# Kernel tuning notes

Measured on AMD Instinct MI355X. Metric: run time of the kernel, lower is better.

## Reference

```python
import jax, jax.numpy as jnp
import numpy as np

N = 16384      # nodes
E = 262144     # edges (avg degree 16)
R = 9          # relation types
D_IN = 384     # embed_size
D_H = 768      # hidden_size
N_CLASSES = 5


def setup_inputs() -> dict:
    key = jax.random.key(0)
    ks = jax.random.split(key, 11)
    s = 0.02
    return {
        "x": jax.random.normal(ks[0], (N, D_IN), jnp.float32),
        "edge_index": jax.random.randint(ks[1], (2, E), 0, N, dtype=jnp.int64)
        if jax.config.jax_enable_x64 else jax.random.randint(ks[1], (2, E), 0, N).astype(jnp.int32),
        "edge_type": jax.random.randint(ks[2], (E,), 0, R).astype(jnp.int32),
        "rel_W": jax.random.normal(ks[3], (R, D_H, D_IN), jnp.float32) * s,
        "rel_b": jax.random.normal(ks[4], (R, D_H), jnp.float32) * s,
        "norm_constants": jnp.ones((R,), jnp.float32),
        "mp_lin_W": jax.random.normal(ks[5], (D_H, D_H), jnp.float32) * s,
        "mp_lin_b": jax.random.normal(ks[6], (D_H,), jnp.float32) * s,
        "mp_self_W": jax.random.normal(ks[7], (D_H, D_H), jnp.float32) * s,
        "mp_self_b": jax.random.normal(ks[8], (D_H,), jnp.float32) * s,
        "out_W": jax.random.normal(ks[9], (N_CLASSES, D_H), jnp.float32) * s,
        "out_b": jax.random.normal(ks[10], (N_CLASSES,), jnp.float32) * s,
    }


def reference(x, edge_index, edge_type, rel_W, rel_b, norm_constants,
              mp_lin_W, mp_lin_b, mp_self_W, mp_self_b, out_W, out_b):
    n = x.shape[0]
    src = edge_index[0]  # j : message source (x_j)
    dst = edge_index[1]  # i : aggregation target

    # --- RelationAwareMP ---
    # edge_weights[i, j] from x @ x.T, computed per edge (identical math)
    ew = jnp.einsum('ed,ed->e', x[dst], x[src])                  # [E]
    norm = ew / norm_constants[edge_type]                        # [E]
    # per-relation linear applied to all nodes, then gathered per edge
    h = jnp.einsum('nd,rhd->rnh', x, rel_W) + rel_b[:, None, :]  # [R,N,H]
    msg = h[edge_type, src]                                      # [E,H]
    aggr = jax.ops.segment_sum(norm[:, None] * msg, dst, num_segments=n)
    x1 = jax.nn.relu(aggr)                                       # [N,H]

    # --- MP (add aggregation + self transform) ---
    self_x = x1 @ mp_self_W.T + mp_self_b
    hm = x1 @ mp_lin_W.T + mp_lin_b
    aggr2 = jax.ops.segment_sum(hm[src], dst, num_segments=n)
    x2 = jax.nn.relu(aggr2 + self_x)                             # [N,H]

    # --- readout ---
    pooled = x2.mean(axis=0)                                     # [H]
    return pooled @ out_W.T + out_b                              # [N_CLASSES]
```

## Files before the change

kernel.cpp:

```cpp
#include <hip/hip_runtime.h>

typedef unsigned char  u8;
typedef unsigned short u16;
typedef unsigned int   u32;

#define NN   16384
#define EE   262144
#define RR   9
#define DIN  384
#define DH   768
#define KSU  3456
#define KS   3488
#define NPB  8
#define PCOP 16

typedef float  f32x4 __attribute__((ext_vector_type(4)));
typedef float  f32x2 __attribute__((ext_vector_type(2)));
typedef __bf16 b16x8 __attribute__((ext_vector_type(8)));

__device__ __forceinline__ u16 f2bf(float f){
  u32 u = __builtin_bit_cast(u32, f);
  u += 0x7fffu + ((u >> 16) & 1u);
  return (u16)(u >> 16);
}
__device__ __forceinline__ float bf2f(u16 h){
  u32 u = ((u32)h) << 16;
  return __builtin_bit_cast(float, u);
}
__device__ __forceinline__ void gll16(const void* g, void* l){
  __builtin_amdgcn_global_load_lds((const __attribute__((address_space(1))) void*)g,
                                   (__attribute__((address_space(3))) void*)l, 16, 0, 0);
}

__global__ void k_count(const int* __restrict__ dst, int* __restrict__ counts){
  const int e = blockIdx.x*256 + threadIdx.x;
  if (e < EE) atomicAdd(&counts[dst[e]], 1);
}

__global__ __launch_bounds__(1024) void k_scan(const int* __restrict__ counts,
                                               int* __restrict__ starts,
                                               int* __restrict__ cursor){
  __shared__ int tot[1024];
  const int t = threadIdx.x;
  int loc[16]; int s = 0;
  #pragma unroll
  for (int j=0;j<16;j++){ loc[j] = counts[t*16+j]; s += loc[j]; }
  tot[t] = s;
  __syncthreads();
  for (int o=1;o<1024;o<<=1){
    int v = (t>=o) ? tot[t-o] : 0;
    __syncthreads();
    tot[t] += v;
    __syncthreads();
  }
  int run = tot[t] - s;
  #pragma unroll
  for (int j=0;j<16;j++){ starts[t*16+j] = run; cursor[t*16+j] = run; run += loc[j]; }
  if (t == 1023) starts[NN] = run;
}

__global__ void k_place(const int* __restrict__ src, const int* __restrict__ dst,
                        const int* __restrict__ et, int* __restrict__ cursor,
                        int* __restrict__ srcp, int* __restrict__ rp){
  const int e = blockIdx.x*256 + threadIdx.x;
  if (e < EE){
    const int p = atomicAdd(&cursor[dst[e]], 1);
    srcp[p] = src[e];
    rp[p]   = et[e];
  }
}

__global__ void k_convW1(const float* __restrict__ rW, const float* __restrict__ rb,
                         u16* __restrict__ Wst){
  const int hh = blockIdx.y;
  const int k  = blockIdx.x*256 + threadIdx.x;
  if (k >= KS) return;
  float v;
  if (k < KSU){ const int r = k / DIN; const int d = k - r*DIN;
                v = rW[((long)r*DH + hh)*DIN + d]; }
  else if (k < KSU + RR){ const int r = k - KSU; v = rb[(long)r*DH + hh]; }
  else v = 0.f;
  Wst[(long)hh*KS + k] = f2bf(v);
}

__global__ void k_convW2(const float* __restrict__ lW, const float* __restrict__ sW,
                         u16* __restrict__ WB){
  const int idx = blockIdx.x*256 + threadIdx.x;
  const float v = (idx < DH*DH) ? lW[idx] : sW[idx - DH*DH];
  WB[idx] = f2bf(v);
}

__global__ __launch_bounds__(256, 3) void k_phase1f(const float* __restrict__ x,
                                                    const int* __restrict__ srcp,
                                                    const int* __restrict__ rp,
                                                    const float* __restrict__ nc,
                                                    const int* __restrict__ starts,
                                                    u16* __restrict__ s){
  const int wv = threadIdx.x >> 6;
  const int l  = threadIdx.x & 63;
  const int i  = blockIdx.x*4 + wv;
  const float* xdp = x + (long)i*DIN;
  const f32x2 xd0 = *(const f32x2*)(xdp + 2*l);
  const f32x2 xd1 = *(const f32x2*)(xdp + 128 + 2*l);
  const f32x2 xd2 = *(const f32x2*)(xdp + 256 + 2*l);
  float acc[RR][6];
  float cacc[RR];
  #pragma unroll
  for (int r=0;r<RR;r++){
    cacc[r] = 0.f;
    #pragma unroll
    for (int j=0;j<6;j++) acc[r][j] = 0.f;
  }
  const int e0 = starts[i], e1 = starts[i+1];
  f32x2 A0={0.f,0.f}, A1={0.f,0.f}, A2={0.f,0.f};
  f32x2 B0={0.f,0.f}, B1={0.f,0.f}, B2={0.f,0.f};
  int rA = 0, rB = 0;
  if (e0 < e1){
    const float* xs = x + (long)srcp[e0]*DIN;
    A0 = *(const f32x2*)(xs + 2*l);
    A1 = *(const f32x2*)(xs + 128 + 2*l);
    A2 = *(const f32x2*)(xs + 256 + 2*l);
    rA = rp[e0];
  }
  if (e0+1 < e1){
    const float* xs = x + (long)srcp[e0+1]*DIN;
    B0 = *(const f32x2*)(xs + 2*l);
    B1 = *(const f32x2*)(xs + 128 + 2*l);
    B2 = *(const f32x2*)(xs + 256 + 2*l);
    rB = rp[e0+1];
  }
  for (int p=e0; p<e1; p+=2){
    const f32x2 a0=A0, a1=A1, a2=A2;
    const f32x2 b0=B0, b1=B1, b2=B2;
    const int ra = rA, rb = rB;
    const bool hb = (p+1 < e1);
    if (p+2 < e1){
      const float* xs = x + (long)srcp[p+2]*DIN;
      A0 = *(const f32x2*)(xs + 2*l);
      A1 = *(const f32x2*)(xs + 128 + 2*l);
      A2 = *(const f32x2*)(xs + 256 + 2*l);
      rA = rp[p+2];
    }
    if (p+3 < e1){
      const float* xs = x + (long)srcp[p+3]*DIN;
      B0 = *(const f32x2*)(xs + 2*l);
      B1 = *(const f32x2*)(xs + 128 + 2*l);
      B2 = *(const f32x2*)(xs + 256 + 2*l);
      rB = rp[p+3];
    }
    float pa = xd0.x*a0.x + xd0.y*a0.y + xd1.x*a1.x + xd1.y*a1.y
             + xd2.x*a2.x + xd2.y*a2.y;
    float pb = xd0.x*b0.x + xd0.y*b0.y + xd1.x*b1.x + xd1.y*b1.y
             + xd2.x*b2.x + xd2.y*b2.y;
    #pragma unroll
    for (int o=32;o;o>>=1){
      pa += __shfl_xor(pa, o);
      pb += __shfl_xor(pb, o);
    }
    #define UPD(R,P,c0,c1,c2) { cacc[R] += P; \
      acc[R][0] += P*c0.x; acc[R][1] += P*c0.y; acc[R][2] += P*c1.x; \
      acc[R][3] += P*c1.y; acc[R][4] += P*c2.x; acc[R][5] += P*c2.y; }
    switch (ra){
      case 0: UPD(0,pa,a0,a1,a2); break; case 1: UPD(1,pa,a0,a1,a2); break;
      case 2: UPD(2,pa,a0,a1,a2); break; case 3: UPD(3,pa,a0,a1,a2); break;
      case 4: UPD(4,pa,a0,a1,a2); break; case 5: UPD(5,pa,a0,a1,a2); break;
      case 6: UPD(6,pa,a0,a1,a2); break; case 7: UPD(7,pa,a0,a1,a2); break;
      default: UPD(8,pa,a0,a1,a2); break;
    }
    if (hb){
      switch (rb){
        case 0: UPD(0,pb,b0,b1,b2); break; case 1: UPD(1,pb,b0,b1,b2); break;
        case 2: UPD(2,pb,b0,b1,b2); break; case 3: UPD(3,pb,b0,b1,b2); break;
        case 4: UPD(4,pb,b0,b1,b2); break; case 5: UPD(5,pb,b0,b1,b2); break;
        case 6: UPD(6,pb,b0,b1,b2); break; case 7: UPD(7,pb,b0,b1,b2); break;
        default: UPD(8,pb,b0,b1,b2); break;
      }
    }
    #undef UPD
  }
  u16* srow = s + (long)i*KS;
  #pragma unroll
  for (int r=0;r<RR;r++){
    const float inv = 1.0f / nc[r];
    #pragma unroll
    for (int seg=0;seg<3;seg++){
      const u32 pk = (u32)f2bf(acc[r][seg*2]*inv)
                   | ((u32)f2bf(acc[r][seg*2+1]*inv) << 16);
      ((u32*)(srow + r*DIN + seg*128))[l] = pk;
    }
  }
  float cv = 0.f;
  #pragma unroll
  for (int r=0;r<RR;r++) cv = (l == r) ? cacc[r] : cv;
  if (l < 32){
    const float invl = (l < RR) ? 1.0f/nc[l] : 0.f;
    srow[KSU + l] = f2bf(l < RR ? cv*invl : 0.f);
  }
}

template<int MODE>
__global__ __launch_bounds__(256, 2)
void k_gemm_bt(const u16* __restrict__ A, const u16* __restrict__ B,
               int M, int N, int K,
               u16* __restrict__ O0, u16* __restrict__ O1,
               const float* __restrict__ b0, const float* __restrict__ b1)
{
  __shared__ __align__(16) u16 As[128*32];
  __shared__ __align__(16) u16 Bs[128*32];
  const int t  = threadIdx.x;
  const int wv = t >> 6;
  const int ln = t & 63;
  const int wm = wv >> 1, wn = wv & 1;
  const long m0 = (long)blockIdx.x * 128;
  const long n0 = (long)blockIdx.y * 128;

  const int srow  = ln >> 2;
  const int skcol = (ln & 3) * 8;

  f32x4 acc[4][4];
  #pragma unroll
  for (int i=0;i<4;i++)
    #pragma unroll
    for (int j=0;j<4;j++) acc[i][j] = {0.f,0.f,0.f,0.f};

  const int fr = ln & 15, fq = ln >> 4;
  const int nk = K >> 5;
  for (int kb=0; kb<nk; ++kb){
    const long k0 = (long)kb * 32;
    #pragma unroll
    for (int q=0;q<2;q++){
      const int seg = wv*2 + q;
      const int row = seg*16 + srow;
      gll16(A + (m0 + row)*(long)K + k0 + skcol, &As[seg*512]);
      gll16(B + (n0 + row)*(long)K + k0 + skcol, &Bs[seg*512]);
    }
    __syncthreads();
    b16x8 av[4], bv[4];
    #pragma unroll
    for (int i=0;i<4;i++){
      av[i] = *(const b16x8*)&As[(wm*64 + i*16 + fr)*32 + fq*8];
      bv[i] = *(const b16x8*)&Bs[(wn*64 + i*16 + fr)*32 + fq*8];
    }
    #pragma unroll
    for (int i=0;i<4;i++)
      #pragma unroll
      for (int j=0;j<4;j++)
        acc[i][j] = __builtin_amdgcn_mfma_f32_16x16x32_bf16(av[i], bv[j], acc[i][j], 0, 0, 0);
    __syncthreads();
  }

  #pragma unroll
  for (int i=0;i<4;i++){
    #pragma unroll
    for (int j=0;j<4;j++){
      #pragma unroll
      for (int r=0;r<4;r++){
        const long m = m0 + wm*64 + i*16 + fq*4 + r;
        const long n = n0 + wn*64 + j*16 + fr;
        float v = acc[i][j][r];
        if (MODE == 0){
          v = v > 0.f ? v : 0.f;
          O0[m*DH + n] = f2bf(v);
        } else {
          if (n < DH) O0[m*DH + n]      = f2bf(v + b0[n]);
          else        O1[m*DH + (n-DH)] = f2bf(v + b1[n-DH]);
        }
      }
    }
  }
}

__global__ __launch_bounds__(128) void k_phase2(const u16* __restrict__ hm,
                                                const u16* __restrict__ sfx,
                                                const int* __restrict__ srcp,
                                                const int* __restrict__ starts,
                                                float* __restrict__ pooledP){
  const int t  = threadIdx.x;
  const int i0 = blockIdx.x * NPB;
  int p = starts[i0];
  const int pend = starts[i0 + NPB];
  u32 C0=0u, C1=0u, C2=0u;
  if (p < pend){
    const u32* hr = (const u32*)(hm + (long)srcp[p]*DH);
    C0 = hr[t]; C1 = hr[t+128]; C2 = hr[t+256];
  }
  float pool[6] = {0.f,0.f,0.f,0.f,0.f,0.f};
  for (int i=i0; i<i0+NPB; ++i){
    const int e1 = starts[i+1];
    float a[6] = {0.f,0.f,0.f,0.f,0.f,0.f};
    while (p < e1){
      const u32 d0=C0, d1=C1, d2=C2;
      if (p+1 < pend){
        const u32* hr = (const u32*)(hm + (long)srcp[p+1]*DH);
        C0 = hr[t]; C1 = hr[t+128]; C2 = hr[t+256];
      }
      a[0] += bf2f((u16)d0); a[1] += bf2f((u16)(d0>>16));
      a[2] += bf2f((u16)d1); a[3] += bf2f((u16)(d1>>16));
      a[4] += bf2f((u16)d2); a[5] += bf2f((u16)(d2>>16));
      ++p;
    }
    const u32* sr = (const u32*)(sfx + (long)i*DH);
    const u32 s0 = sr[t], s1 = sr[t+128], s2 = sr[t+256];
    float v;
    v = a[0] + bf2f((u16)s0);        pool[0] += v > 0.f ? v : 0.f;
    v = a[1] + bf2f((u16)(s0>>16));  pool[1] += v > 0.f ? v : 0.f;
    v = a[2] + bf2f((u16)s1);        pool[2] += v > 0.f ? v : 0.f;
    v = a[3] + bf2f((u16)(s1>>16));  pool[3] += v > 0.f ? v : 0.f;
    v = a[4] + bf2f((u16)s2);        pool[4] += v > 0.f ? v : 0.f;
    v = a[5] + bf2f((u16)(s2>>16));  pool[5] += v > 0.f ? v : 0.f;
  }
  float* pd = pooledP + (blockIdx.x & (PCOP-1)) * DH;
  atomicAdd(&pd[2*t],       pool[0]);
  atomicAdd(&pd[2*t+1],     pool[1]);
  atomicAdd(&pd[256+2*t],   pool[2]);
  atomicAdd(&pd[256+2*t+1], pool[3]);
  atomicAdd(&pd[512+2*t],   pool[4]);
  atomicAdd(&pd[512+2*t+1], pool[5]);
}

__global__ __launch_bounds__(256) void k_final(const float* __restrict__ pooledP,
                                               const float* __restrict__ oW,
                                               const float* __restrict__ ob,
                                               float* __restrict__ out){
  __shared__ float ps[DH];
  __shared__ float red[256];
  const int t = threadIdx.x;
  for (int h=t; h<DH; h+=256){
    float s = 0.f;
    #pragma unroll
    for (int c=0;c<PCOP;c++) s += pooledP[c*DH + h];
    ps[h] = s;
  }
  __syncthreads();
  for (int c=0;c<5;c++){
    float p = 0.f;
    for (int h=t; h<DH; h+=256) p += ps[h]*oW[c*DH + h];
    red[t] = p; __syncthreads();
    for (int o=128;o;o>>=1){ if (t<o) red[t]+=red[t+o]; __syncthreads(); }
    if (t == 0) out[c] = red[0]*(1.f/(float)NN) + ob[c];
    __syncthreads();
  }
}

extern "C" void kernel_launch(void* const* d_in, const int* in_sizes, int n_in,
                              void* d_out, int out_size, void* d_ws, size_t ws_size,
                              hipStream_t stream)
{
  (void)in_sizes; (void)n_in; (void)out_size; (void)ws_size;
  const float* x     = (const float*)d_in[0];
  const int*   ei    = (const int*)  d_in[1];
  const int*   et    = (const int*)  d_in[2];
  const float* relW  = (const float*)d_in[3];
  const float* relb  = (const float*)d_in[4];
  const float* nc    = (const float*)d_in[5];
  const float* linW  = (const float*)d_in[6];
  const float* linb  = (const float*)d_in[7];
  const float* selfW = (const float*)d_in[8];
  const float* selfb = (const float*)d_in[9];
  const float* outW  = (const float*)d_in[10];
  const float* outb  = (const float*)d_in[11];
  float* out = (float*)d_out;

  u8* w = (u8*)d_ws;
  int*   counts = (int*)(w + 0);
  int*   starts = (int*)(w + 65536);
  int*   cursor = (int*)(w + 131328);
  int*   srcp   = (int*)(w + 196864);
  int*   rp     = (int*)(w + 2294016);
  u16*   Wst    = (u16*)(w + 4391168);
  u16*   WB     = (u16*)(w + 9748736);
  u16*   x1     = (u16*)(w + 12108032);
  u16*   S      = (u16*)(w + 37276928);
  u16*   hm     = S;
  u16*   sfx    = (u16*)(w + 37276928 + 25165824);
  float* pooledP = (float*)(w + 37276928 + 50331648);

  const int* esrc = ei;
  const int* edst = ei + EE;

  hipMemsetAsync(counts, 0, NN*sizeof(int), stream);

  k_count <<<EE/256, 256, 0, stream>>>(edst, counts);
  k_scan  <<<1, 1024, 0, stream>>>(counts, starts, cursor);
  k_place <<<EE/256, 256, 0, stream>>>(esrc, edst, et, cursor, srcp, rp);
  k_convW1<<<dim3(14, DH), 256, 0, stream>>>(relW, relb, Wst);
  k_convW2<<<(2*DH*DH)/256, 256, 0, stream>>>(linW, selfW, WB);
  k_phase1f<<<NN/4, 256, 0, stream>>>(x, srcp, rp, nc, starts, S);
  k_gemm_bt<0><<<dim3(NN/128, DH/128), 256, 0, stream>>>(
      S, Wst, NN, DH, KS, x1, (u16*)nullptr, (const float*)nullptr, (const float*)nullptr);
  hipMemsetAsync(pooledP, 0, PCOP*DH*sizeof(float), stream);
  k_gemm_bt<1><<<dim3(NN/128, 2*DH/128), 256, 0, stream>>>(
      x1, WB, NN, 2*DH, DH, hm, sfx, linb, selfb);
  k_phase2<<<NN/NPB, 128, 0, stream>>>(hm, sfx, srcp, starts, pooledP);
  k_final <<<1, 256, 0, stream>>>(pooledP, outW, outb, out);
}
```

Before: 494.9 us.

## Pack edge src/type, deepen gather prefetch, DPP reductions, swap GEMM grid order

Packs each edge's source index and relation type into one int, which halves the CSR index reads. The phase-1 gather now prefetches four edges ahead and reduces its dot products with DPP and ds_swizzle instead of a full shuffle chain. Phase 2 now handles four nodes per block and runs an eight-deep prefetch pipeline across node boundaries. The GEMM grid is transposed so that N tiles vary fastest, which should improve reuse of A tiles in L2, and its occupancy hint is raised to 3. The extra prefetch depth raises register pressure, and the packing assumes the source index fits in 14 bits and the relation type in 4.

```diff
diff --git a/kernel.cpp b/kernel.cpp
--- a/kernel.cpp
+++ b/kernel.cpp
@@ -11,7 +11,7 @@
 #define DH   768
 #define KSU  3456
 #define KS   3488
-#define NPB  8
+#define NPB  4
 #define PCOP 16
 
 typedef float  f32x4 __attribute__((ext_vector_type(4)));
@@ -30,6 +30,14 @@
 __device__ __forceinline__ void gll16(const void* g, void* l){
   __builtin_amdgcn_global_load_lds((const __attribute__((address_space(1))) void*)g,
                                    (__attribute__((address_space(3))) void*)l, 16, 0, 0);
+}
+template<int N> __device__ __forceinline__ float dppror(float v){
+  return __builtin_bit_cast(float,
+    __builtin_amdgcn_update_dpp(0, __builtin_bit_cast(int, v), 0x120+N, 0xF, 0xF, true));
+}
+__device__ __forceinline__ float swz16(float v){
+  return __builtin_bit_cast(float,
+    __builtin_amdgcn_ds_swizzle(__builtin_bit_cast(int, v), 0x401F));
 }
 
 __global__ void k_count(const int* __restrict__ dst, int* __restrict__ counts){
@@ -61,12 +69,11 @@
 
 __global__ void k_place(const int* __restrict__ src, const int* __restrict__ dst,
                         const int* __restrict__ et, int* __restrict__ cursor,
-                        int* __restrict__ srcp, int* __restrict__ rp){
+                        int* __restrict__ sp){
   const int e = blockIdx.x*256 + threadIdx.x;
   if (e < EE){
     const int p = atomicAdd(&cursor[dst[e]], 1);
-    srcp[p] = src[e];
-    rp[p]   = et[e];
+    sp[p] = (int)(((u32)et[e] << 28) | (u32)src[e]);
   }
 }
 
@@ -91,8 +98,7 @@
 }
 
 __global__ __launch_bounds__(256, 3) void k_phase1f(const float* __restrict__ x,
-                                                    const int* __restrict__ srcp,
-                                                    const int* __restrict__ rp,
+                                                    const int* __restrict__ sp,
                                                     const float* __restrict__ nc,
                                                     const int* __restrict__ starts,
                                                     u16* __restrict__ s){
@@ -112,72 +118,52 @@
     for (int j=0;j<6;j++) acc[r][j] = 0.f;
   }
   const int e0 = starts[i], e1 = starts[i+1];
-  f32x2 A0={0.f,0.f}, A1={0.f,0.f}, A2={0.f,0.f};
-  f32x2 B0={0.f,0.f}, B1={0.f,0.f}, B2={0.f,0.f};
-  int rA = 0, rB = 0;
-  if (e0 < e1){
-    const float* xs = x + (long)srcp[e0]*DIN;
-    A0 = *(const f32x2*)(xs + 2*l);
-    A1 = *(const f32x2*)(xs + 128 + 2*l);
-    A2 = *(const f32x2*)(xs + 256 + 2*l);
-    rA = rp[e0];
-  }
-  if (e0+1 < e1){
-    const float* xs = x + (long)srcp[e0+1]*DIN;
-    B0 = *(const f32x2*)(xs + 2*l);
-    B1 = *(const f32x2*)(xs + 128 + 2*l);
-    B2 = *(const f32x2*)(xs + 256 + 2*l);
-    rB = rp[e0+1];
-  }
-  for (int p=e0; p<e1; p+=2){
-    const f32x2 a0=A0, a1=A1, a2=A2;
-    const f32x2 b0=B0, b1=B1, b2=B2;
-    const int ra = rA, rb = rB;
-    const bool hb = (p+1 < e1);
-    if (p+2 < e1){
-      const float* xs = x + (long)srcp[p+2]*DIN;
-      A0 = *(const f32x2*)(xs + 2*l);
-      A1 = *(const f32x2*)(xs + 128 + 2*l);
-      A2 = *(const f32x2*)(xs + 256 + 2*l);
-      rA = rp[p+2];
-    }
-    if (p+3 < e1){
-      const float* xs = x + (long)srcp[p+3]*DIN;
-      B0 = *(const f32x2*)(xs + 2*l);
-      B1 = *(const f32x2*)(xs + 128 + 2*l);
-      B2 = *(const f32x2*)(xs + 256 + 2*l);
-      rB = rp[p+3];
-    }
-    float pa = xd0.x*a0.x + xd0.y*a0.y + xd1.x*a1.x + xd1.y*a1.y
-             + xd2.x*a2.x + xd2.y*a2.y;
-    float pb = xd0.x*b0.x + xd0.y*b0.y + xd1.x*b1.x + xd1.y*b1.y
-             + xd2.x*b2.x + xd2.y*b2.y;
-    #pragma unroll
-    for (int o=32;o;o>>=1){
-      pa += __shfl_xor(pa, o);
-      pb += __shfl_xor(pb, o);
-    }
-    #define UPD(R,P,c0,c1,c2) { cacc[R] += P; \
+  f32x2 Aa={0.f,0.f},Ab={0.f,0.f},Ac={0.f,0.f};
+  f32x2 Ba={0.f,0.f},Bb={0.f,0.f},Bc={0.f,0.f};
+  f32x2 Ca={0.f,0.f},Cb={0.f,0.f},Cc={0.f,0.f};
+  f32x2 Da={0.f,0.f},Db={0.f,0.f},Dc={0.f,0.f};
+  u32 qA=0,qB=0,qC=0,qD=0;
+  #define LDE(S, QQ, IDX) { const int pe_=(IDX); if (pe_ < e1){ QQ = (u32)sp[pe_]; \
+      const float* xs_ = x + (long)(QQ & 0x3FFFu)*DIN; \
+      S##a = *(const f32x2*)(xs_ + 2*l); \
+      S##b = *(const f32x2*)(xs_ + 128 + 2*l); \
+      S##c = *(const f32x2*)(xs_ + 256 + 2*l); } }
+  LDE(A,qA,e0) LDE(B,qB,e0+1) LDE(C,qC,e0+2) LDE(D,qD,e0+3)
+  #define DOT(u0,u1,u2) (xd0.x*u0.x + xd0.y*u0.y + xd1.x*u1.x + xd1.y*u1.y \
+                       + xd2.x*u2.x + xd2.y*u2.y)
+  #define UPD(R,P,c0,c1,c2) { cacc[R] += P; \
       acc[R][0] += P*c0.x; acc[R][1] += P*c0.y; acc[R][2] += P*c1.x; \
       acc[R][3] += P*c1.y; acc[R][4] += P*c2.x; acc[R][5] += P*c2.y; }
-    switch (ra){
-      case 0: UPD(0,pa,a0,a1,a2); break; case 1: UPD(1,pa,a0,a1,a2); break;
-      case 2: UPD(2,pa,a0,a1,a2); break; case 3: UPD(3,pa,a0,a1,a2); break;
-      case 4: UPD(4,pa,a0,a1,a2); break; case 5: UPD(5,pa,a0,a1,a2); break;
-      case 6: UPD(6,pa,a0,a1,a2); break; case 7: UPD(7,pa,a0,a1,a2); break;
-      default: UPD(8,pa,a0,a1,a2); break;
-    }
-    if (hb){
-      switch (rb){
-        case 0: UPD(0,pb,b0,b1,b2); break; case 1: UPD(1,pb,b0,b1,b2); break;
-        case 2: UPD(2,pb,b0,b1,b2); break; case 3: UPD(3,pb,b0,b1,b2); break;
-        case 4: UPD(4,pb,b0,b1,b2); break; case 5: UPD(5,pb,b0,b1,b2); break;
-        case 6: UPD(6,pb,b0,b1,b2); break; case 7: UPD(7,pb,b0,b1,b2); break;
-        default: UPD(8,pb,b0,b1,b2); break;
-      }
-    }
-    #undef UPD
-  }
+  #define SW(RQ,P,c0,c1,c2) switch (RQ){ \
+      case 0: UPD(0,P,c0,c1,c2); break; case 1: UPD(1,P,c0,c1,c2); break; \
+      case 2: UPD(2,P,c0,c1,c2); break; case 3: UPD(3,P,c0,c1,c2); break; \
+      case 4: UPD(4,P,c0,c1,c2); break; case 5: UPD(5,P,c0,c1,c2); break; \
+      case 6: UPD(6,P,c0,c1,c2); break; case 7: UPD(7,P,c0,c1,c2); break; \
+      default: UPD(8,P,c0,c1,c2); break; }
+  for (int p=e0; p<e1; p+=4){
+    const f32x2 a0=Aa,a1=Ab,a2=Ac, b0=Ba,b1=Bb,b2=Bc;
+    const f32x2 c0=Ca,c1=Cb,c2=Cc, d0=Da,d1=Db,d2=Dc;
+    const u32 qa=qA, qb=qB, qc=qC, qd=qD;
+    const bool h1 = p+1<e1, h2 = p+2<e1, h3 = p+3<e1;
+    LDE(A,qA,p+4) LDE(B,qB,p+5) LDE(C,qC,p+6) LDE(D,qD,p+7)
+    float pa = DOT(a0,a1,a2), pb = DOT(b0,b1,b2);
+    float pc = DOT(c0,c1,c2), pd = DOT(d0,d1,d2);
+    pa += dppror<1>(pa); pb += dppror<1>(pb); pc += dppror<1>(pc); pd += dppror<1>(pd);
+    pa += dppror<2>(pa); pb += dppror<2>(pb); pc += dppror<2>(pc); pd += dppror<2>(pd);
+    pa += dppror<4>(pa); pb += dppror<4>(pb); pc += dppror<4>(pc); pd += dppror<4>(pd);
+    pa += dppror<8>(pa); pb += dppror<8>(pb); pc += dppror<8>(pc); pd += dppror<8>(pd);
+    pa += swz16(pa); pb += swz16(pb); pc += swz16(pc); pd += swz16(pd);
+    pa += __shfl_xor(pa,32); pb += __shfl_xor(pb,32);
+    pc += __shfl_xor(pc,32); pd += __shfl_xor(pd,32);
+    SW(qa>>28, pa, a0,a1,a2);
+    if (h1){ SW(qb>>28, pb, b0,b1,b2); }
+    if (h2){ SW(qc>>28, pc, c0,c1,c2); }
+    if (h3){ SW(qd>>28, pd, d0,d1,d2); }
+  }
+  #undef LDE
+  #undef DOT
+  #undef UPD
+  #undef SW
   u16* srow = s + (long)i*KS;
   #pragma unroll
   for (int r=0;r<RR;r++){
@@ -199,7 +185,7 @@
 }
 
 template<int MODE>
-__global__ __launch_bounds__(256, 2)
+__global__ __launch_bounds__(256, 3)
 void k_gemm_bt(const u16* __restrict__ A, const u16* __restrict__ B,
                int M, int N, int K,
                u16* __restrict__ O0, u16* __restrict__ O1,
@@ -211,8 +197,8 @@
   const int wv = t >> 6;
   const int ln = t & 63;
   const int wm = wv >> 1, wn = wv & 1;
-  const long m0 = (long)blockIdx.x * 128;
-  const long n0 = (long)blockIdx.y * 128;
+  const long m0 = (long)blockIdx.y * 128;
+  const long n0 = (long)blockIdx.x * 128;
 
   const int srow  = ln >> 2;
   const int skcol = (ln & 3) * 8;
@@ -272,50 +258,64 @@
 
 __global__ __launch_bounds__(128) void k_phase2(const u16* __restrict__ hm,
                                                 const u16* __restrict__ sfx,
-                                                const int* __restrict__ srcp,
+                                                const int* __restrict__ sp,
                                                 const int* __restrict__ starts,
                                                 float* __restrict__ pooledP){
   const int t  = threadIdx.x;
   const int i0 = blockIdx.x * NPB;
-  int p = starts[i0];
+  const int p0 = starts[i0];
   const int pend = starts[i0 + NPB];
-  u32 C0=0u, C1=0u, C2=0u;
-  if (p < pend){
-    const u32* hr = (const u32*)(hm + (long)srcp[p]*DH);
-    C0 = hr[t]; C1 = hr[t+128]; C2 = hr[t+256];
-  }
-  float pool[6] = {0.f,0.f,0.f,0.f,0.f,0.f};
-  for (int i=i0; i<i0+NPB; ++i){
-    const int e1 = starts[i+1];
-    float a[6] = {0.f,0.f,0.f,0.f,0.f,0.f};
-    while (p < e1){
-      const u32 d0=C0, d1=C1, d2=C2;
-      if (p+1 < pend){
-        const u32* hr = (const u32*)(hm + (long)srcp[p+1]*DH);
-        C0 = hr[t]; C1 = hr[t+128]; C2 = hr[t+256];
-      }
-      a[0] += bf2f((u16)d0); a[1] += bf2f((u16)(d0>>16));
-      a[2] += bf2f((u16)d1); a[3] += bf2f((u16)(d1>>16));
-      a[4] += bf2f((u16)d2); a[5] += bf2f((u16)(d2>>16));
-      ++p;
-    }
-    const u32* sr = (const u32*)(sfx + (long)i*DH);
-    const u32 s0 = sr[t], s1 = sr[t+128], s2 = sr[t+256];
-    float v;
-    v = a[0] + bf2f((u16)s0);        pool[0] += v > 0.f ? v : 0.f;
-    v = a[1] + bf2f((u16)(s0>>16));  pool[1] += v > 0.f ? v : 0.f;
-    v = a[2] + bf2f((u16)s1);        pool[2] += v > 0.f ? v : 0.f;
-    v = a[3] + bf2f((u16)(s1>>16));  pool[3] += v > 0.f ? v : 0.f;
-    v = a[4] + bf2f((u16)s2);        pool[4] += v > 0.f ? v : 0.f;
-    v = a[5] + bf2f((u16)(s2>>16));  pool[5] += v > 0.f ? v : 0.f;
-  }
+  u32 sf00,sf01,sf02, sf10,sf11,sf12, sf20,sf21,sf22, sf30,sf31,sf32;
+  { const u32* sr = (const u32*)(sfx + (long)(i0+0)*DH); sf00=sr[t]; sf01=sr[t+128]; sf02=sr[t+256]; }
+  { const u32* sr = (const u32*)(sfx + (long)(i0+1)*DH); sf10=sr[t]; sf11=sr[t+128]; sf12=sr[t+256]; }
+  { const u32* sr = (const u32*)(sfx + (long)(i0+2)*DH); sf20=sr[t]; sf21=sr[t+128]; sf22=sr[t+256]; }
+  { const u32* sr = (const u32*)(sfx + (long)(i0+3)*DH); sf30=sr[t]; sf31=sr[t+128]; sf32=sr[t+256]; }
+  u32 A0=0,A1=0,A2=0,B0=0,B1=0,B2=0,C0=0,C1=0,C2=0,D0=0,D1=0,D2=0;
+  u32 E0=0,E1=0,E2=0,F0=0,F1=0,F2=0,G0=0,G1=0,G2=0,H0=0,H1=0,H2=0;
+  #define PLD(S, IDX) { const int nf_=(IDX); if (nf_ < pend){ \
+      const u32* hr_ = (const u32*)(hm + (long)(((u32)sp[nf_]) & 0x3FFFu)*DH); \
+      S##0=hr_[t]; S##1=hr_[t+128]; S##2=hr_[t+256]; } }
+  PLD(A,p0)   PLD(B,p0+1) PLD(C,p0+2) PLD(D,p0+3)
+  PLD(E,p0+4) PLD(F,p0+5) PLD(G,p0+6) PLD(H,p0+7)
+  float a0=0.f,a1=0.f,a2=0.f,a3=0.f,a4=0.f,a5=0.f;
+  float q0=0.f,q1=0.f,q2=0.f,q3=0.f,q4=0.f,q5=0.f;
+  int i = i0;
+  int e1 = starts[i0+1];
+  #define FLUSH(K) { float v_; \
+    v_=a0+bf2f((u16)sf##K##0);        q0+=fmaxf(v_,0.f); \
+    v_=a1+bf2f((u16)(sf##K##0>>16));  q1+=fmaxf(v_,0.f); \
+    v_=a2+bf2f((u16)sf##K##1);        q2+=fmaxf(v_,0.f); \
+    v_=a3+bf2f((u16)(sf##K##1>>16));  q3+=fmaxf(v_,0.f); \
+    v_=a4+bf2f((u16)sf##K##2);        q4+=fmaxf(v_,0.f); \
+    v_=a5+bf2f((u16)(sf##K##2>>16));  q5+=fmaxf(v_,0.f); \
+    a0=a1=a2=a3=a4=a5=0.f; }
+  #define FLUSHI { switch (i - i0){ case 0: FLUSH(0); break; case 1: FLUSH(1); break; \
+                   case 2: FLUSH(2); break; default: FLUSH(3); break; } }
+  while (i < i0+NPB && e1 == p0){ FLUSHI; ++i; e1 = (i < i0+NPB) ? starts[i+1] : 0x7fffffff; }
+  #define STEP(S, K) { const int pe_ = base + K; if (pe_ < pend){ \
+      const u32 d0_=S##0, d1_=S##1, d2_=S##2; \
+      PLD(S, pe_ + 8); \
+      a0+=bf2f((u16)d0_); a1+=bf2f((u16)(d0_>>16)); \
+      a2+=bf2f((u16)d1_); a3+=bf2f((u16)(d1_>>16)); \
+      a4+=bf2f((u16)d2_); a5+=bf2f((u16)(d2_>>16)); \
+      while (i < i0+NPB && pe_+1 == e1){ FLUSHI; ++i; \
+        e1 = (i < i0+NPB) ? starts[i+1] : 0x7fffffff; } } }
+  for (int base = p0; base < pend; base += 8){
+    STEP(A,0) STEP(B,1) STEP(C,2) STEP(D,3)
+    STEP(E,4) STEP(F,5) STEP(G,6) STEP(H,7)
+  }
+  while (i < i0+NPB){ FLUSHI; ++i; }
+  #undef PLD
+  #undef FLUSH
+  #undef FLUSHI
+  #undef STEP
   float* pd = pooledP + (blockIdx.x & (PCOP-1)) * DH;
-  atomicAdd(&pd[2*t],       pool[0]);
-  atomicAdd(&pd[2*t+1],     pool[1]);
-  atomicAdd(&pd[256+2*t],   pool[2]);
-  atomicAdd(&pd[256+2*t+1], pool[3]);
-  atomicAdd(&pd[512+2*t],   pool[4]);
-  atomicAdd(&pd[512+2*t+1], pool[5]);
+  atomicAdd(&pd[2*t],       q0);
+  atomicAdd(&pd[2*t+1],     q1);
+  atomicAdd(&pd[256+2*t],   q2);
+  atomicAdd(&pd[256+2*t+1], q3);
+  atomicAdd(&pd[512+2*t],   q4);
+  atomicAdd(&pd[512+2*t+1], q5);
 }
 
 __global__ __launch_bounds__(256) void k_final(const float* __restrict__ pooledP,
@@ -366,7 +366,6 @@
   int*   starts = (int*)(w + 65536);
   int*   cursor = (int*)(w + 131328);
   int*   srcp   = (int*)(w + 196864);
-  int*   rp     = (int*)(w + 2294016);
   u16*   Wst    = (u16*)(w + 4391168);
   u16*   WB     = (u16*)(w + 9748736);
   u16*   x1     = (u16*)(w + 12108032);
@@ -382,14 +381,14 @@
 
   k_count <<<EE/256, 256, 0, stream>>>(edst, counts);
   k_scan  <<<1, 1024, 0, stream>>>(counts, starts, cursor);
-  k_place <<<EE/256, 256, 0, stream>>>(esrc, edst, et, cursor, srcp, rp);
+  k_place <<<EE/256, 256, 0, stream>>>(esrc, edst, et, cursor, srcp);
   k_convW1<<<dim3(14, DH), 256, 0, stream>>>(relW, relb, Wst);
   k_convW2<<<(2*DH*DH)/256, 256, 0, stream>>>(linW, selfW, WB);
-  k_phase1f<<<NN/4, 256, 0, stream>>>(x, srcp, rp, nc, starts, S);
-  k_gemm_bt<0><<<dim3(NN/128, DH/128), 256, 0, stream>>>(
+  k_phase1f<<<NN/4, 256, 0, stream>>>(x, srcp, nc, starts, S);
+  k_gemm_bt<0><<<dim3(DH/128, NN/128), 256, 0, stream>>>(
       S, Wst, NN, DH, KS, x1, (u16*)nullptr, (const float*)nullptr, (const float*)nullptr);
   hipMemsetAsync(pooledP, 0, PCOP*DH*sizeof(float), stream);
-  k_gemm_bt<1><<<dim3(NN/128, 2*DH/128), 256, 0, stream>>>(
+  k_gemm_bt<1><<<dim3(2*DH/128, NN/128), 256, 0, stream>>>(
       x1, WB, NN, 2*DH, DH, hm, sfx, linb, selfb);
   k_phase2<<<NN/NPB, 128, 0, stream>>>(hm, sfx, srcp, starts, pooledP);
   k_final <<<1, 256, 0, stream>>>(pooledP, outW, outb, out);
```

After: 476.8 us. 1.04x faster.
